# Kernel tuning notes

Measured on AMD Instinct MI355X. Metric: run time of the kernel, lower is better.

The kernel has to match this reference:

```python
import jax, jax.numpy as jnp
import numpy as np

ACT_BITS = 8
W_BITS = 8
C_IN = 64


def round_ste(x):
    # straight-through rounding (Brevitas training behavior)
    return x + jax.lax.stop_gradient(jnp.round(x) - x)


def fake_quant(x, scale, bits, signed):
    if signed:
        lo, hi = -(2 ** (bits - 1)), 2 ** (bits - 1) - 1
    else:
        lo, hi = 0, 2 ** bits - 1
    return jnp.clip(round_ste(x / scale), lo, hi) * scale


def conv_nchw(x, w, pad, groups=1):
    return jax.lax.conv_general_dilated(
        x, w, window_strides=(1, 1), padding=((pad, pad), (pad, pad)),
        dimension_numbers=("NCHW", "OIHW", "NCHW"), feature_group_count=groups)


def setup_inputs() -> dict:
    key = jax.random.key(0)
    k0, k1, k2, k3 = jax.random.split(key, 4)
    x = jax.random.normal(k0, (8, 64, 112, 112), jnp.float32)
    w1 = jax.random.normal(k1, (64, 1, 3, 3), jnp.float32) * 0.05    # depthwise 3x3
    w2 = jax.random.normal(k2, (128, 64, 1, 1), jnp.float32) * 0.05  # pointwise 1x1
    w_sc = jax.random.normal(k3, (128, 64, 1, 1), jnp.float32) * 0.05  # shortcut 1x1
    sc = lambda v: jnp.asarray(v, jnp.float32)
    return dict(x=x, w1=w1, w2=w2, w_sc=w_sc,
                s_in=sc(0.03), s_relu=sc(0.02), s_add=sc(0.03),
                sw1=sc(0.004), sw2=sc(0.004), sw_sc=sc(0.004))


def reference(x, w1, w2, w_sc, s_in, s_relu, s_add, sw1, sw2, sw_sc):
    # quant_input: signed 8-bit fake-quant of the activation
    xq = fake_quant(x, s_in, ACT_BITS, True)
    # shortcut: 1x1 conv with int8 fake-quantized weights (inplane != ouplane)
    identity = conv_nchw(xq, fake_quant(w_sc, sw_sc, W_BITS, True), pad=0)
    # conv1: depthwise 3x3 (groups=inplane) with int8 fake-quantized weights
    y = conv_nchw(xq, fake_quant(w1, sw1, W_BITS, True), pad=1, groups=C_IN)
    # relu2: QuantReLU -> unsigned 8-bit fake-quant of relu
    y = fake_quant(jax.nn.relu(y), s_relu, ACT_BITS, False)
    # conv2: pointwise 1x1
    y = conv_nchw(y, fake_quant(w2, sw2, W_BITS, True), pad=0)
    # residual_add: add then requantize to signed 8-bit
    return fake_quant(y + identity, s_add, ACT_BITS, True)
```

## Files before the change

kernel.cpp:

```cpp
#include <hip/hip_runtime.h>
#include <hip/hip_bf16.h>
#include <stdint.h>

#define NIMG 8
#define CIN  64
#define HWI  12544
#define COUT 128

typedef short v8s __attribute__((ext_vector_type(8)));
typedef float v4f __attribute__((ext_vector_type(4)));

static __device__ __forceinline__ int q8(float x, float inv, float lo, float hi) {
    float t = rintf(x * inv);
    t = fminf(fmaxf(t, lo), hi);
    return (int)t;
}

static __device__ __forceinline__ uint32_t funnel(uint32_t hi, uint32_t lo, int sh) {
    return (uint32_t)(((((uint64_t)hi) << 32) | (uint64_t)lo) >> sh);
}

static __device__ __forceinline__ int dot4(uint32_t a, uint32_t b, int c) {
    int acc = c;
    #pragma unroll
    for (int i = 0; i < 4; ++i)
        acc += (int)(int8_t)(a >> (8*i)) * (int)(int8_t)(b >> (8*i));
    return acc;
}

static __device__ __forceinline__ uint16_t i2bf(int v) {
    union { float f; uint32_t u; } c; c.f = (float)v;
    return (uint16_t)(c.u >> 16);
}

__global__ void __launch_bounds__(256) wprep_kernel(
    const float* __restrict__ w2, const float* __restrict__ wsc,
    const float* __restrict__ sw2p, const float* __restrict__ swscp,
    uint16_t* __restrict__ wbuf)
{
    int t = blockIdx.x * 256 + threadIdx.x;
    int f = t * 4;
    int co = f >> 6, k = f & 63;
    float inv2 = 1.0f / sw2p[0];
    float invs = 1.0f / swscp[0];
    float4 a = *(const float4*)(w2 + f);
    float4 b = *(const float4*)(wsc + f);
    float av[4] = {a.x, a.y, a.z, a.w};
    float bv[4] = {b.x, b.y, b.z, b.w};
    uint16_t* d2 = wbuf + co*128 + k;
    uint16_t* ds = wbuf + co*128 + 64 + k;
    *(ushort2*)(d2)     = make_ushort2(i2bf(q8(av[0], inv2, -128.f, 127.f)),
                                       i2bf(q8(av[1], inv2, -128.f, 127.f)));
    *(ushort2*)(d2 + 2) = make_ushort2(i2bf(q8(av[2], inv2, -128.f, 127.f)),
                                       i2bf(q8(av[3], inv2, -128.f, 127.f)));
    *(ushort2*)(ds)     = make_ushort2(i2bf(q8(bv[0], invs, -128.f, 127.f)),
                                       i2bf(q8(bv[1], invs, -128.f, 127.f)));
    *(ushort2*)(ds + 2) = make_ushort2(i2bf(q8(bv[2], invs, -128.f, 127.f)),
                                       i2bf(q8(bv[3], invs, -128.f, 127.f)));
}

__global__ void __launch_bounds__(256) fused_kernel(
    const float* __restrict__ x, const float* __restrict__ w1,
    const uint16_t* __restrict__ wbuf,
    const float* __restrict__ sinp, const float* __restrict__ srelup,
    const float* __restrict__ saddp, const float* __restrict__ sw1p,
    const float* __restrict__ sw2p, const float* __restrict__ swscp,
    float* __restrict__ out)
{
    __shared__ int8_t   tile[64 * 348];
    __shared__ uint16_t Bl[112 * 136];

    int bid = blockIdx.x;
    int n = bid / 112, h = bid - n*112;
    int tid = threadIdx.x;
    int wave = tid >> 6, lane = tid & 63;
    int lr = lane >> 4, ln = lane & 15;
    float sin_f = sinp[0];
    float inv_sin = 1.0f / sin_f;

    for (int i = 0; i < 21; ++i) {
        int id = tid + i*256;
        int c = id / 84; int rem = id - c*84;
        int r = rem / 28; int seg = rem - r*28;
        int grow = h + r - 1;
        float4 v = make_float4(0.f, 0.f, 0.f, 0.f);
        if ((unsigned)grow < 112u)
            v = *(const float4*)(x + ((size_t)(n*64 + c) * HWI + grow*112 + seg*4));
        float vv[4] = {v.x, v.y, v.z, v.w};
        uint32_t pk = 0;
        #pragma unroll
        for (int e = 0; e < 4; ++e) {
            int q = q8(vv[e], inv_sin, -128.0f, 127.0f);
            pk |= (uint32_t)(q & 255) << (8*e);
        }
        *(uint32_t*)&tile[c*348 + r*116 + seg*4] = pk;
    }
    if (tid < 192) {
        int c = tid / 3, r = tid - c*3;
        *(uint32_t*)&tile[c*348 + r*116 + 112] = 0;
    }
    __syncthreads();

    {
        int c = lane;
        int w0b = wave * 28;

        float isw1 = 1.0f / sw1p[0];
        uint32_t wp[3];
        #pragma unroll
        for (int ky = 0; ky < 3; ++ky) {
            uint32_t pk = 0;
            #pragma unroll
            for (int kx = 0; kx < 3; ++kx) {
                int q = q8(w1[c*9 + ky*3 + kx], isw1, -128.0f, 127.0f);
                pk |= (uint32_t)(q & 255) << (8*kx);
            }
            wp[ky] = pk;
        }
        float r1 = (sin_f * sw1p[0]) / srelup[0];

        int base[3];
        #pragma unroll
        for (int r2 = 0; r2 < 3; ++r2) base[r2] = c*348 + r2*116;

        uint32_t Ar[3], Br[3], Cr[3];
        #pragma unroll
        for (int r2 = 0; r2 < 3; ++r2) {
            Ar[r2] = wave ? *(uint32_t*)&tile[base[r2] + w0b - 4] : 0u;
            Br[r2] = *(uint32_t*)&tile[base[r2] + w0b];
            Cr[r2] = *(uint32_t*)&tile[base[r2] + w0b + 4];
        }

        for (int q = 0; q < 7; ++q) {
            int acc0 = 0, acc1 = 0, acc2 = 0, acc3 = 0;
            #pragma unroll
            for (int r2 = 0; r2 < 3; ++r2) {
                uint32_t d0 = funnel(Br[r2], Ar[r2], 24);
                uint32_t d1 = Br[r2];
                uint32_t d2 = funnel(Cr[r2], Br[r2], 8);
                uint32_t d3 = funnel(Cr[r2], Br[r2], 16);
                acc0 = dot4(d0, wp[r2], acc0);
                acc1 = dot4(d1, wp[r2], acc1);
                acc2 = dot4(d2, wp[r2], acc2);
                acc3 = dot4(d3, wp[r2], acc3);
            }
            int accs[4] = {acc0, acc1, acc2, acc3};
            uint32_t xdw = Br[1];
            int pxb = w0b + q*4;
            #pragma unroll
            for (int j = 0; j < 4; ++j) {
                float t = rintf((float)accs[j] * r1);
                t = fminf(fmaxf(t, 0.0f), 255.0f);
                int xv = (int)(int8_t)((xdw >> (8*j)) & 255);
                Bl[(pxb + j)*136 + c]      = i2bf((int)t);
                Bl[(pxb + j)*136 + 64 + c] = i2bf(xv);
            }
            #pragma unroll
            for (int r2 = 0; r2 < 3; ++r2) { Ar[r2] = Br[r2]; Br[r2] = Cr[r2]; }
            if (q < 6) {
                #pragma unroll
                for (int r2 = 0; r2 < 3; ++r2)
                    Cr[r2] = *(uint32_t*)&tile[base[r2] + w0b + q*4 + 8];
            }
        }
    }
    __syncthreads();

    {
        float S2  = sw2p[0] * srelup[0];
        float Ssc = swscp[0] * sinp[0];
        float sadd = saddp[0];
        float inv_sadd = 1.0f / sadd;

        v8s a[2][4];
        #pragma unroll
        for (int mi = 0; mi < 2; ++mi) {
            int m = (wave*2 + mi)*16 + ln;
            #pragma unroll
            for (int seg = 0; seg < 4; ++seg)
                a[mi][seg] = *(const v8s*)(wbuf + (size_t)m*128 + seg*32 + lr*8);
        }

        size_t orow = (size_t)n*COUT*HWI + (size_t)h*112;

        for (int nt = 0; nt < 7; ++nt) {
            int boff = (nt*16 + ln)*136 + lr*8;
            v8s bf[4];
            #pragma unroll
            for (int seg = 0; seg < 4; ++seg)
                bf[seg] = *(const v8s*)&Bl[boff + seg*32];
            #pragma unroll
            for (int mi = 0; mi < 2; ++mi) {
                v4f acc2 = {0.f, 0.f, 0.f, 0.f};
                v4f accs = {0.f, 0.f, 0.f, 0.f};
                acc2 = __builtin_amdgcn_mfma_f32_16x16x32_bf16(a[mi][0], bf[0], acc2, 0, 0, 0);
                acc2 = __builtin_amdgcn_mfma_f32_16x16x32_bf16(a[mi][1], bf[1], acc2, 0, 0, 0);
                accs = __builtin_amdgcn_mfma_f32_16x16x32_bf16(a[mi][2], bf[2], accs, 0, 0, 0);
                accs = __builtin_amdgcn_mfma_f32_16x16x32_bf16(a[mi][3], bf[3], accs, 0, 0, 0);
                size_t obase = orow + (size_t)((wave*2 + mi)*16 + lr*4)*HWI + nt*16 + ln;
                #pragma unroll
                for (int r = 0; r < 4; ++r) {
                    float v = S2 * acc2[r] + Ssc * accs[r];
                    float t = rintf(v * inv_sadd);
                    t = fminf(fmaxf(t, -128.0f), 127.0f);
                    out[obase + (size_t)r*HWI] = t * sadd;
                }
            }
        }
    }
}

extern "C" void kernel_launch(void* const* d_in, const int* in_sizes, int n_in,
                              void* d_out, int out_size, void* d_ws, size_t ws_size,
                              hipStream_t stream) {
    const float* x     = (const float*)d_in[0];
    const float* w1    = (const float*)d_in[1];
    const float* w2    = (const float*)d_in[2];
    const float* wsc   = (const float*)d_in[3];
    const float* sin   = (const float*)d_in[4];
    const float* srelu = (const float*)d_in[5];
    const float* sadd  = (const float*)d_in[6];
    const float* sw1   = (const float*)d_in[7];
    const float* sw2   = (const float*)d_in[8];
    const float* swsc  = (const float*)d_in[9];

    uint16_t* wbuf = (uint16_t*)d_ws;

    wprep_kernel<<<8, 256, 0, stream>>>(w2, wsc, sw2, swsc, wbuf);
    fused_kernel<<<NIMG * 112, 256, 0, stream>>>(x, w1, wbuf,
                                                 sin, srelu, sadd, sw1, sw2, swsc,
                                                 (float*)d_out);
}
```

Measured before the change: 122.3 us.

## Batch input loads, hoist weight loads, prefetch B fragments, raise occupancy hint

All 21 float4 global loads of the input tile are now issued before any quantization, so many requests are in flight at once instead of load-quantize-store per iteration. The depthwise and MFMA weight loads are moved to the kernel start so their latency overlaps the input fetch. The B fragments from LDS are double-buffered across the pointwise tile loop, the depthwise loop is fully unrolled, and launch bounds now request 3 blocks per CU. Holding 21 float4 values plus the hoisted weights raises register pressure, and the occupancy hint may force spills.

```diff
diff --git a/kernel.cpp b/kernel.cpp
--- a/kernel.cpp
+++ b/kernel.cpp
@@ -59,7 +59,7 @@
                                        i2bf(q8(bv[3], invs, -128.f, 127.f)));
 }
 
-__global__ void __launch_bounds__(256) fused_kernel(
+__global__ void __launch_bounds__(256, 3) fused_kernel(
     const float* __restrict__ x, const float* __restrict__ w1,
     const uint16_t* __restrict__ wbuf,
     const float* __restrict__ sinp, const float* __restrict__ srelup,
@@ -78,45 +78,62 @@
     float sin_f = sinp[0];
     float inv_sin = 1.0f / sin_f;
 
+    int c = lane;
+    float isw1 = 1.0f / sw1p[0];
+    uint32_t wp[3];
+    #pragma unroll
+    for (int ky = 0; ky < 3; ++ky) {
+        uint32_t pk = 0;
+        #pragma unroll
+        for (int kx = 0; kx < 3; ++kx) {
+            int q = q8(w1[c*9 + ky*3 + kx], isw1, -128.0f, 127.0f);
+            pk |= (uint32_t)(q & 255) << (8*kx);
+        }
+        wp[ky] = pk;
+    }
+
+    v8s a[2][4];
+    #pragma unroll
+    for (int mi = 0; mi < 2; ++mi) {
+        int m = (wave*2 + mi)*16 + ln;
+        #pragma unroll
+        for (int seg = 0; seg < 4; ++seg)
+            a[mi][seg] = *(const v8s*)(wbuf + (size_t)m*128 + seg*32 + lr*8);
+    }
+
+    float4 vals[21];
+    #pragma unroll
     for (int i = 0; i < 21; ++i) {
         int id = tid + i*256;
-        int c = id / 84; int rem = id - c*84;
+        int cc = id / 84; int rem = id - cc*84;
         int r = rem / 28; int seg = rem - r*28;
         int grow = h + r - 1;
-        float4 v = make_float4(0.f, 0.f, 0.f, 0.f);
+        vals[i] = make_float4(0.f, 0.f, 0.f, 0.f);
         if ((unsigned)grow < 112u)
-            v = *(const float4*)(x + ((size_t)(n*64 + c) * HWI + grow*112 + seg*4));
-        float vv[4] = {v.x, v.y, v.z, v.w};
+            vals[i] = *(const float4*)(x + ((size_t)(n*64 + cc) * HWI + grow*112 + seg*4));
+    }
+    #pragma unroll
+    for (int i = 0; i < 21; ++i) {
+        int id = tid + i*256;
+        int cc = id / 84; int rem = id - cc*84;
+        int r = rem / 28; int seg = rem - r*28;
+        float vv[4] = {vals[i].x, vals[i].y, vals[i].z, vals[i].w};
         uint32_t pk = 0;
         #pragma unroll
         for (int e = 0; e < 4; ++e) {
             int q = q8(vv[e], inv_sin, -128.0f, 127.0f);
             pk |= (uint32_t)(q & 255) << (8*e);
         }
-        *(uint32_t*)&tile[c*348 + r*116 + seg*4] = pk;
+        *(uint32_t*)&tile[cc*348 + r*116 + seg*4] = pk;
     }
     if (tid < 192) {
-        int c = tid / 3, r = tid - c*3;
-        *(uint32_t*)&tile[c*348 + r*116 + 112] = 0;
+        int cc = tid / 3, r = tid - cc*3;
+        *(uint32_t*)&tile[cc*348 + r*116 + 112] = 0;
     }
     __syncthreads();
 
     {
-        int c = lane;
         int w0b = wave * 28;
-
-        float isw1 = 1.0f / sw1p[0];
-        uint32_t wp[3];
-        #pragma unroll
-        for (int ky = 0; ky < 3; ++ky) {
-            uint32_t pk = 0;
-            #pragma unroll
-            for (int kx = 0; kx < 3; ++kx) {
-                int q = q8(w1[c*9 + ky*3 + kx], isw1, -128.0f, 127.0f);
-                pk |= (uint32_t)(q & 255) << (8*kx);
-            }
-            wp[ky] = pk;
-        }
         float r1 = (sin_f * sw1p[0]) / srelup[0];
 
         int base[3];
@@ -131,6 +148,7 @@
             Cr[r2] = *(uint32_t*)&tile[base[r2] + w0b + 4];
         }
 
+        #pragma unroll
         for (int q = 0; q < 7; ++q) {
             int acc0 = 0, acc1 = 0, acc2 = 0, acc3 = 0;
             #pragma unroll
@@ -172,23 +190,24 @@
         float sadd = saddp[0];
         float inv_sadd = 1.0f / sadd;
 
-        v8s a[2][4];
-        #pragma unroll
-        for (int mi = 0; mi < 2; ++mi) {
-            int m = (wave*2 + mi)*16 + ln;
-            #pragma unroll
-            for (int seg = 0; seg < 4; ++seg)
-                a[mi][seg] = *(const v8s*)(wbuf + (size_t)m*128 + seg*32 + lr*8);
-        }
-
         size_t orow = (size_t)n*COUT*HWI + (size_t)h*112;
 
-        for (int nt = 0; nt < 7; ++nt) {
-            int boff = (nt*16 + ln)*136 + lr*8;
-            v8s bf[4];
+        v8s bf[4];
+        {
+            int boff = ln*136 + lr*8;
             #pragma unroll
             for (int seg = 0; seg < 4; ++seg)
                 bf[seg] = *(const v8s*)&Bl[boff + seg*32];
+        }
+
+        for (int nt = 0; nt < 7; ++nt) {
+            v8s bfn[4];
+            if (nt < 6) {
+                int boff = ((nt+1)*16 + ln)*136 + lr*8;
+                #pragma unroll
+                for (int seg = 0; seg < 4; ++seg)
+                    bfn[seg] = *(const v8s*)&Bl[boff + seg*32];
+            }
             #pragma unroll
             for (int mi = 0; mi < 2; ++mi) {
                 v4f acc2 = {0.f, 0.f, 0.f, 0.f};
@@ -205,6 +224,10 @@
                     t = fminf(fmaxf(t, -128.0f), 127.0f);
                     out[obase + (size_t)r*HWI] = t * sadd;
                 }
+            }
+            if (nt < 6) {
+                #pragma unroll
+                for (int seg = 0; seg < 4; ++seg) bf[seg] = bfn[seg];
             }
         }
     }
```

Measured after the change: 128.8 us. 1.05x slower.
